# Performance work log

Hardware: AMD Instinct MI355X
Metric: run time of the kernel (lower is better)

The kernel has to match this reference:

```python
import jax, jax.numpy as jnp
import numpy as np
import math

B, C, T = 4, 512, 2048
H = 8            # num_heads
G = 32           # GroupNorm groups (GroupNorm32 in ADM-style code)
EPS = 1e-5


def setup_inputs() -> dict:
    key = jax.random.key(0)
    ks = jax.random.split(key, 7)
    x = jax.random.normal(ks[0], (B, C, T), jnp.float32)
    norm_scale = 1.0 + 0.02 * jax.random.normal(ks[1], (C,), jnp.float32)
    norm_bias = 0.02 * jax.random.normal(ks[2], (C,), jnp.float32)
    qkv_w = 0.02 * jax.random.normal(ks[3], (3 * C, C), jnp.float32)  # 1x1 conv == matmul
    qkv_b = 0.02 * jax.random.normal(ks[4], (3 * C,), jnp.float32)
    proj_w = 0.02 * jax.random.normal(ks[5], (C, C), jnp.float32)
    proj_b = 0.02 * jax.random.normal(ks[6], (C,), jnp.float32)
    return {"x": x, "norm_scale": norm_scale, "norm_bias": norm_bias,
            "qkv_w": qkv_w, "qkv_b": qkv_b, "proj_w": proj_w, "proj_b": proj_b}


def _group_norm(x, scale, bias):
    # x: [B, C, T]; 32-group norm over (C/G, T) per group
    b, c, t = x.shape
    xg = x.reshape(b, G, (c // G) * t)
    mean = jnp.mean(xg, axis=-1, keepdims=True)
    var = jnp.var(xg, axis=-1, keepdims=True)
    xg = (xg - mean) * jax.lax.rsqrt(var + EPS)
    return xg.reshape(b, c, t) * scale[None, :, None] + bias[None, :, None]


def reference(x, norm_scale, norm_bias, qkv_w, qkv_b, proj_w, proj_b):
    b, c, t = x.shape
    ch = c // H
    h = _group_norm(x, norm_scale, norm_bias)
    qkv = jnp.einsum('oc,bct->bot', qkv_w, h) + qkv_b[None, :, None]  # [B, 3C, T]
    q, k, v = jnp.split(qkv, 3, axis=1)
    q = q.reshape(b * H, ch, t)
    k = k.reshape(b * H, ch, t)
    v = v.reshape(b * H, ch, t)
    scale = 1.0 / math.sqrt(math.sqrt(ch))
    w = jnp.einsum('bct,bcs->bts', q * scale, k * scale)              # [B*H, T, T]
    w = jax.nn.softmax(w.astype(jnp.float32), axis=-1).astype(qkv.dtype)
    a = jnp.einsum('bts,bcs->bct', w, v).reshape(b, c, t)             # [B, C, T]
    out = jnp.einsum('oc,bct->bot', proj_w, a) + proj_b[None, :, None]
    return x + out
```

## Files before the change

### kernel.cpp

```cpp
#include <hip/hip_runtime.h>

typedef short bf16x8 __attribute__((ext_vector_type(8)));
typedef float f32x4 __attribute__((ext_vector_type(4)));
typedef float f32x16 __attribute__((ext_vector_type(16)));
typedef unsigned short u16;
typedef unsigned int u32;

constexpr int B = 4, C = 512, T = 2048, H = 8, G = 32;
constexpr int CH = C / H;
constexpr int CPG = C / G;
constexpr float EPS = 1e-5f;
constexpr float SCLQ = 0.18033688011112042f;

__device__ __forceinline__ u16 f2bf(float f) {
  union { float f; u32 u; } v; v.f = f;
  return (u16)((v.u + 0x7FFFu + ((v.u >> 16) & 1u)) >> 16);
}

__device__ __forceinline__ u32 cvtpk(float lo, float hi) {
  u32 r;
  asm("v_cvt_pk_bf16_f32 %0, %1, %2" : "=v"(r) : "v"(lo), "v"(hi));
  return r;
}

__device__ __forceinline__ void gload16(const void* g, void* lds) {
  __builtin_amdgcn_global_load_lds(
      (const __attribute__((address_space(1))) void*)g,
      (__attribute__((address_space(3))) void*)lds, 16, 0, 0);
}

__device__ __forceinline__ void pl32swap(u32& a, u32& b) {
  asm("v_permlane32_swap_b32 %0, %1" : "+v"(a), "+v"(b));
}

template <int ROWS>
__device__ __forceinline__ void stage_swz_8w(u16* lds, const u16* gsrc, int ldk) {
  const int tid = threadIdx.x;
  const int w = tid >> 6, lane = tid & 63;
#pragma unroll
  for (int i = 0; i < ROWS / 64; ++i) {
    const int chunk = i * 8 + w;
    const int row = chunk * 8 + (lane >> 3);
    const int col = ((lane & 7) * 8) ^ ((row & 7) << 3);
    gload16(gsrc + (size_t)row * ldk + col, (char*)lds + chunk * 1024);
  }
}

__global__ __launch_bounds__(256) void prep_k(const float* __restrict__ x,
                                              float* __restrict__ stats,
                                              const float* __restrict__ s1,
                                              u16* __restrict__ d1, int n1,
                                              const float* __restrict__ s2,
                                              u16* __restrict__ d2, int n2) {
  __shared__ float red[8];
  const int bid = blockIdx.x;
  if (bid >= 128) {
    int i = (bid - 128) * 256 + threadIdx.x;
    const float4* src = (const float4*)s1;
    uint2* dst = (uint2*)d1;
    float scl = (i < 65536) ? SCLQ : 1.0f;
    if (i >= n1) { i -= n1; scl = 1.0f; if (i >= n2) return; src = (const float4*)s2; dst = (uint2*)d2; }
    float4 v = src[i];
    uint2 pk;
    pk.x = cvtpk(v.x * scl, v.y * scl);
    pk.y = cvtpk(v.z * scl, v.w * scl);
    dst[i] = pk;
    return;
  }
  const int bg = bid;
  const float4* xp = (const float4*)(x + (size_t)bg * CPG * T);
  float s = 0.f, ss = 0.f;
  for (int i = threadIdx.x; i < CPG * T / 4; i += 256) {
    float4 v = xp[i];
    s += v.x + v.y + v.z + v.w;
    ss += v.x * v.x + v.y * v.y + v.z * v.z + v.w * v.w;
  }
  for (int off = 32; off; off >>= 1) {
    s += __shfl_down(s, off);
    ss += __shfl_down(ss, off);
  }
  const int w = threadIdx.x >> 6;
  if ((threadIdx.x & 63) == 0) { red[w] = s; red[4 + w] = ss; }
  __syncthreads();
  if (threadIdx.x == 0) {
    float S = red[0] + red[1] + red[2] + red[3];
    float SS = red[4] + red[5] + red[6] + red[7];
    const float inv = 1.f / (float)(CPG * T);
    float mean = S * inv;
    float var = SS * inv - mean * mean;
    stats[bg * 2] = mean;
    stats[bg * 2 + 1] = rsqrtf(var + EPS);
  }
}

__global__ __launch_bounds__(256) void gn_apply_k(const float* __restrict__ x,
                                                  const float* __restrict__ stats,
                                                  const float* __restrict__ gsc,
                                                  const float* __restrict__ gbi,
                                                  u16* __restrict__ ht) {
  const int b = blockIdx.y;
  const int t0 = blockIdx.x * 16;
#pragma unroll
  for (int p = 0; p < 2; ++p) {
    const int c = p * 256 + threadIdx.x;
    const int bg = b * G + (c >> 4);
    const float mean = stats[bg * 2], rstd = stats[bg * 2 + 1];
    const float sc = gsc[c] * rstd;
    const float bi = gbi[c] - mean * sc;
    const float4* xp = (const float4*)(x + ((size_t)b * C + c) * T + t0);
#pragma unroll
    for (int j = 0; j < 4; ++j) {
      float4 v = xp[j];
      const int t = t0 + j * 4;
      u16* hp = ht + ((size_t)b * T + t) * C + c;
      hp[0]     = f2bf(v.x * sc + bi);
      hp[C]     = f2bf(v.y * sc + bi);
      hp[2 * C] = f2bf(v.z * sc + bi);
      hp[3 * C] = f2bf(v.w * sc + bi);
    }
  }
}

__global__ __launch_bounds__(512, 2) void qkv_gemm_k(const u16* __restrict__ ht,
                                                     const u16* __restrict__ wq,
                                                     const float* __restrict__ qkvb,
                                                     u16* __restrict__ qo,
                                                     u16* __restrict__ kvo_k,
                                                     u16* __restrict__ kvo_v) {
  __shared__ u16 As[2][128 * 64];
  __shared__ u16 Bs[2][128 * 64];
  const int bid = blockIdx.x;
  const int wg = (bid & 7) * 96 + (bid >> 3);
  const int nt = wg % 12;
  const int mtb = wg / 12;
  const int mt = mtb & 15, b = mtb >> 4;
  const u16* Ab = ht + ((size_t)b * T + mt * 128) * C;
  const u16* Bb = wq + (size_t)nt * 128 * C;
  const int tid = threadIdx.x, lane = tid & 63, w = tid >> 6;
  const int wr = w >> 1, wc = w & 1, l15 = lane & 15, lhi = lane >> 4;
  const int swz = (l15 & 7) << 3;
  constexpr int NK = C / 64;

  const f32x4 vzero = {0.f, 0.f, 0.f, 0.f};
  f32x4 acc[2][4];
#pragma unroll
  for (int m = 0; m < 2; ++m)
#pragma unroll
    for (int n = 0; n < 4; ++n) acc[m][n] = vzero;

  stage_swz_8w<128>(As[0], Ab, C);
  stage_swz_8w<128>(Bs[0], Bb, C);
  asm volatile("s_waitcnt vmcnt(0)" ::: "memory");
  __builtin_amdgcn_s_barrier();
  asm volatile("" ::: "memory");

  int cur = 0;
  for (int kt = 0; kt < NK; ++kt) {
    if (kt + 1 < NK) {
      stage_swz_8w<128>(As[cur ^ 1], Ab + (kt + 1) * 64, C);
      stage_swz_8w<128>(Bs[cur ^ 1], Bb + (kt + 1) * 64, C);
    }
#pragma unroll
    for (int kk = 0; kk < 2; ++kk) {
      const int koff = (kk * 32 + lhi * 8) ^ swz;
      bf16x8 af[2], bfv[4];
#pragma unroll
      for (int m = 0; m < 2; ++m)
        af[m] = *(const bf16x8*)&As[cur][(wr * 32 + m * 16 + l15) * 64 + koff];
#pragma unroll
      for (int n = 0; n < 4; ++n)
        bfv[n] = *(const bf16x8*)&Bs[cur][(wc * 64 + n * 16 + l15) * 64 + koff];
#pragma unroll
      for (int m = 0; m < 2; ++m)
#pragma unroll
        for (int n = 0; n < 4; ++n)
          acc[m][n] = __builtin_amdgcn_mfma_f32_16x16x32_bf16(af[m], bfv[n], acc[m][n], 0, 0, 0);
    }
    if (kt + 1 < NK) {
      asm volatile("s_waitcnt vmcnt(0)" ::: "memory");
      __builtin_amdgcn_s_barrier();
      asm volatile("" ::: "memory");
    }
    cur ^= 1;
  }
#pragma unroll
  for (int n = 0; n < 4; ++n) {
    const int o = nt * 128 + wc * 64 + n * 16 + l15;
    const int which = o >> 9, rem = o & 511, hh = rem >> 6, d = rem & 63;
    const float bias = (which == 0) ? qkvb[o] * SCLQ : qkvb[o];
    const size_t bh = (size_t)b * H + hh;
#pragma unroll
    for (int m = 0; m < 2; ++m) {
      const int tbase = mt * 128 + wr * 32 + m * 16 + lhi * 4;
      const u32 w01 = cvtpk(acc[m][n][0] + bias, acc[m][n][1] + bias);
      const u32 w23 = cvtpk(acc[m][n][2] + bias, acc[m][n][3] + bias);
      if (which == 2) {
        uint2 pk; pk.x = w01; pk.y = w23;
        *(uint2*)&kvo_v[(bh * CH + d) * T + tbase] = pk;
      } else {
        u16* dst = (which == 0) ? qo : kvo_k;
        dst[(bh * T + tbase) * CH + d]     = (u16)(w01 & 0xffff);
        dst[(bh * T + tbase + 1) * CH + d] = (u16)(w01 >> 16);
        dst[(bh * T + tbase + 2) * CH + d] = (u16)(w23 & 0xffff);
        dst[(bh * T + tbase + 3) * CH + d] = (u16)(w23 >> 16);
      }
    }
  }
}

__global__ __launch_bounds__(512, 4) void attn_k(const u16* __restrict__ q,
                                                 const u16* __restrict__ k,
                                                 const u16* __restrict__ v,
                                                 u16* __restrict__ at) {
  __shared__ u16 Ks[2][128 * 64];
  __shared__ u16 Vs[2][2][64 * 64];
  const int lin = blockIdx.x + (blockIdx.y << 4);
  const int wg = (lin & 7) * 64 + (lin >> 3);
  const int qt = wg & 15, bh = wg >> 4;
  const int tid = threadIdx.x, lane = tid & 63, w = tid >> 6;
  const int qset = w & 3, grp = w >> 2;
  const int l31 = lane & 31, h = lane >> 5;
  const u16* qb = q + (size_t)bh * T * CH;
  const u16* kb = k + (size_t)bh * T * CH;
  const u16* vb = v + (size_t)bh * CH * T;
  constexpr int NP = T / 128;

  bf16x8 qf[4];
  {
    const u16* qp = qb + (size_t)(qt * 128 + qset * 32 + l31) * CH + h * 8;
#pragma unroll
    for (int ks = 0; ks < 4; ++ks) qf[ks] = *(const bf16x8*)(qp + ks * 16);
  }
  union { u32 u[4]; bf16x8 v8; } ones;
#pragma unroll
  for (int i = 0; i < 4; ++i) ones.u[i] = 0x3F803F80u;

  stage_swz_8w<128>(Ks[0], kb, CH);
  stage_swz_8w<64>(Vs[0][0], vb, T);
  stage_swz_8w<64>(Vs[0][1], vb + 64, T);
  asm volatile("s_waitcnt vmcnt(0)" ::: "memory");
  __builtin_amdgcn_s_barrier();
  asm volatile("" ::: "memory");

  f32x16 accO0 = {0.f,0.f,0.f,0.f,0.f,0.f,0.f,0.f,0.f,0.f,0.f,0.f,0.f,0.f,0.f,0.f};
  f32x16 accO1 = accO0;
  f32x16 accL = accO0;
  const int kswz = (l31 & 7) << 3;

  int cur = 0;
  for (int p = 0; p < NP; ++p) {
    if (p + 1 < NP) {
      stage_swz_8w<128>(Ks[cur ^ 1], kb + (size_t)(p + 1) * 128 * CH, CH);
      stage_swz_8w<64>(Vs[cur ^ 1][0], vb + (p + 1) * 128, T);
      stage_swz_8w<64>(Vs[cur ^ 1][1], vb + (p + 1) * 128 + 64, T);
    }
    const u16* Kc = &Ks[cur][grp * 64 * 64];
    const u16* Vc = Vs[cur][grp];

    f32x16 accS0 = {0.f,0.f,0.f,0.f,0.f,0.f,0.f,0.f,0.f,0.f,0.f,0.f,0.f,0.f,0.f,0.f};
    f32x16 accS1 = accS0;
    __builtin_amdgcn_s_setprio(1);
#pragma unroll
    for (int ks = 0; ks < 4; ++ks) {
      const int col = (ks * 16 + h * 8) ^ kswz;
      bf16x8 kf0 = *(const bf16x8*)&Kc[l31 * 64 + col];
      bf16x8 kf1 = *(const bf16x8*)&Kc[(32 + l31) * 64 + col];
      accS0 = __builtin_amdgcn_mfma_f32_32x32x16_bf16(kf0, qf[ks], accS0, 0, 0, 0);
      accS1 = __builtin_amdgcn_mfma_f32_32x32x16_bf16(kf1, qf[ks], accS1, 0, 0, 0);
    }
    __builtin_amdgcn_s_setprio(0);

    u32 wd0[8], wd1[8];
#pragma unroll
    for (int i = 0; i < 8; ++i) {
      float pa = __builtin_amdgcn_exp2f(accS0[2 * i]);
      float pb = __builtin_amdgcn_exp2f(accS0[2 * i + 1]);
      asm("v_cvt_pk_bf16_f32 %0, %1, %2" : "=v"(wd0[i]) : "v"(pa), "v"(pb));
    }
#pragma unroll
    for (int i = 0; i < 8; ++i) {
      float pa = __builtin_amdgcn_exp2f(accS1[2 * i]);
      float pb = __builtin_amdgcn_exp2f(accS1[2 * i + 1]);
      asm("v_cvt_pk_bf16_f32 %0, %1, %2" : "=v"(wd1[i]) : "v"(pa), "v"(pb));
    }
    pl32swap(wd0[0], wd0[2]); pl32swap(wd0[1], wd0[3]);
    pl32swap(wd0[4], wd0[6]); pl32swap(wd0[5], wd0[7]);
    pl32swap(wd1[0], wd1[2]); pl32swap(wd1[1], wd1[3]);
    pl32swap(wd1[4], wd1[6]); pl32swap(wd1[5], wd1[7]);

    __builtin_amdgcn_s_setprio(1);
#pragma unroll
    for (int kt = 0; kt < 2; ++kt) {
      const u32* wd = kt ? wd1 : wd0;
      union { u32 u[4]; bf16x8 v8; } fa, fb;
      fa.u[0] = wd[0]; fa.u[1] = wd[1]; fa.u[2] = wd[2]; fa.u[3] = wd[3];
      fb.u[0] = wd[4]; fb.u[1] = wd[5]; fb.u[2] = wd[6]; fb.u[3] = wd[7];
      const int sA = (kt * 32 + h * 8) ^ kswz;
      const int sB = (kt * 32 + 16 + h * 8) ^ kswz;
      {
        bf16x8 vf0 = *(const bf16x8*)&Vc[l31 * 64 + sA];
        bf16x8 vf1 = *(const bf16x8*)&Vc[l31 * 64 + sB];
        accO0 = __builtin_amdgcn_mfma_f32_32x32x16_bf16(fa.v8, vf0, accO0, 0, 0, 0);
        accO0 = __builtin_amdgcn_mfma_f32_32x32x16_bf16(fb.v8, vf1, accO0, 0, 0, 0);
      }
      {
        bf16x8 vf0 = *(const bf16x8*)&Vc[(32 + l31) * 64 + sA];
        bf16x8 vf1 = *(const bf16x8*)&Vc[(32 + l31) * 64 + sB];
        accO1 = __builtin_amdgcn_mfma_f32_32x32x16_bf16(fa.v8, vf0, accO1, 0, 0, 0);
        accO1 = __builtin_amdgcn_mfma_f32_32x32x16_bf16(fb.v8, vf1, accO1, 0, 0, 0);
      }
      accL = __builtin_amdgcn_mfma_f32_32x32x16_bf16(fa.v8, ones.v8, accL, 0, 0, 0);
      accL = __builtin_amdgcn_mfma_f32_32x32x16_bf16(fb.v8, ones.v8, accL, 0, 0, 0);
    }
    __builtin_amdgcn_s_setprio(0);

    asm volatile("s_waitcnt vmcnt(0)" ::: "memory");
    __builtin_amdgcn_s_barrier();
    asm volatile("" ::: "memory");
    cur ^= 1;
  }

  float* fO = (float*)&Ks[0][0];
  float* fL = (float*)&Vs[0][0][0];
  if (grp == 1) {
#pragma unroll
    for (int r = 0; r < 16; ++r) {
      const int qrow = (r & 3) + 8 * (r >> 2) + 4 * h;
      float* row = fO + (qset * 32 + qrow) * 64;
      row[l31] = accO0[r];
      row[32 + l31] = accO1[r];
      if (l31 == 0) fL[qset * 32 + qrow] = accL[r];
    }
  }
  __syncthreads();
  if (grp == 0) {
    const int bq = bh >> 3, hh = bh & 7;
#pragma unroll
    for (int r = 0; r < 16; ++r) {
      const int qrow = (r & 3) + 8 * (r >> 2) + 4 * h;
      const float denom = accL[r] + fL[qset * 32 + qrow];
      const float invr = __builtin_amdgcn_rcpf(denom);
      const float* row = fO + (qset * 32 + qrow) * 64;
      const float o0 = accO0[r] + row[l31];
      const float o1 = accO1[r] + row[32 + l31];
      const int t = qt * 128 + qset * 32 + qrow;
      u16* op = at + ((size_t)bq * T + t) * C + hh * 64 + l31;
      op[0]  = f2bf(o0 * invr);
      op[32] = f2bf(o1 * invr);
    }
  }
}

__global__ __launch_bounds__(512, 2) void proj_gemm_k(const u16* __restrict__ at,
                                                      const u16* __restrict__ wp,
                                                      const float* __restrict__ pb,
                                                      const float* __restrict__ x,
                                                      float* __restrict__ out) {
  __shared__ u16 As[2][128 * 64];
  __shared__ u16 Bs[2][64 * 64];
  const int bid = blockIdx.x;
  const int wg = (bid & 7) * 64 + (bid >> 3);
  const int nt = wg & 7;
  const int mtb = wg >> 3;
  const int mt = mtb & 15, b = mtb >> 4;
  const u16* Ab = at + ((size_t)b * T + mt * 128) * C;
  const u16* Bb = wp + (size_t)nt * 64 * C;
  const int tid = threadIdx.x, lane = tid & 63, w = tid >> 6;
  const int l15 = lane & 15, lhi = lane >> 4;
  const int swz = (l15 & 7) << 3;
  constexpr int NK = C / 64;

  const f32x4 vzero = {0.f, 0.f, 0.f, 0.f};
  f32x4 acc[4];
#pragma unroll
  for (int n = 0; n < 4; ++n) acc[n] = vzero;

  stage_swz_8w<128>(As[0], Ab, C);
  stage_swz_8w<64>(Bs[0], Bb, C);
  asm volatile("s_waitcnt vmcnt(0)" ::: "memory");
  __builtin_amdgcn_s_barrier();
  asm volatile("" ::: "memory");

  int cur = 0;
  for (int kt = 0; kt < NK; ++kt) {
    if (kt + 1 < NK) {
      stage_swz_8w<128>(As[cur ^ 1], Ab + (kt + 1) * 64, C);
      stage_swz_8w<64>(Bs[cur ^ 1], Bb + (kt + 1) * 64, C);
    }
#pragma unroll
    for (int kk = 0; kk < 2; ++kk) {
      const int koff = (kk * 32 + lhi * 8) ^ swz;
      bf16x8 af = *(const bf16x8*)&As[cur][(w * 16 + l15) * 64 + koff];
      bf16x8 bfv[4];
#pragma unroll
      for (int n = 0; n < 4; ++n)
        bfv[n] = *(const bf16x8*)&Bs[cur][(n * 16 + l15) * 64 + koff];
#pragma unroll
      for (int n = 0; n < 4; ++n)
        acc[n] = __builtin_amdgcn_mfma_f32_16x16x32_bf16(af, bfv[n], acc[n], 0, 0, 0);
    }
    if (kt + 1 < NK) {
      asm volatile("s_waitcnt vmcnt(0)" ::: "memory");
      __builtin_amdgcn_s_barrier();
      asm volatile("" ::: "memory");
    }
    cur ^= 1;
  }
#pragma unroll
  for (int n = 0; n < 4; ++n) {
    const int o = nt * 64 + n * 16 + l15;
    const float bias = pb[o];
    const int tbase = mt * 128 + w * 16 + lhi * 4;
    const size_t idx = ((size_t)b * C + o) * T + tbase;
    const float4 xv = *(const float4*)&x[idx];
    float4 ov;
    ov.x = xv.x + acc[n][0] + bias;
    ov.y = xv.y + acc[n][1] + bias;
    ov.z = xv.z + acc[n][2] + bias;
    ov.w = xv.w + acc[n][3] + bias;
    *(float4*)&out[idx] = ov;
  }
}

extern "C" void kernel_launch(void* const* d_in, const int* in_sizes, int n_in,
                              void* d_out, int out_size, void* d_ws, size_t ws_size,
                              hipStream_t stream) {
  const float* x     = (const float*)d_in[0];
  const float* gsc   = (const float*)d_in[1];
  const float* gbi   = (const float*)d_in[2];
  const float* qkvw  = (const float*)d_in[3];
  const float* qkvb  = (const float*)d_in[4];
  const float* projw = (const float*)d_in[5];
  const float* projb = (const float*)d_in[6];
  float* out = (float*)d_out;

  char* ws = (char*)d_ws;
  float* stats = (float*)ws;
  u16* wq = (u16*)(ws + 1024);
  u16* wp = (u16*)(ws + 1024 + 1572864);
  u16* ht = (u16*)(ws + 2098176);
  u16* qo = (u16*)(ws + 10486784);
  u16* ko = (u16*)(ws + 18875392);
  u16* vo = (u16*)(ws + 27264000);
  u16* at = ht;

  prep_k<<<1152, 256, 0, stream>>>(x, stats, qkvw, wq, 196608, projw, wp, 65536);
  gn_apply_k<<<dim3(T / 16, B), 256, 0, stream>>>(x, stats, gsc, gbi, ht);
  qkv_gemm_k<<<768, 512, 0, stream>>>(ht, wq, qkvb, qo, ko, vo);
  attn_k<<<dim3(T / 128, B * H), 512, 0, stream>>>(qo, ko, vo, at);
  proj_gemm_k<<<512, 512, 0, stream>>>(at, wp, projb, x, out);
}
```

Measured before the change: 104.7 us.

## Software-pipeline QK^T one tile ahead of softmax and PV in attention loop

Restructures the attention main loop so the S=K·Q MFMAs for tile p+1 are issued after the exp/convert of tile p and before the PV MFMAs. K is now prefetched two tiles ahead and V one tile ahead, with a prologue that computes the first S tile. The aim is to overlap the transcendental/VALU softmax work with matrix-core work and keep the MFMA pipe busy. In exchange the S accumulators stay live across iterations, which raises register pressure, and the extra prologue barrier adds a little synchronization.

```diff
diff --git a/kernel.cpp b/kernel.cpp
--- a/kernel.cpp
+++ b/kernel.cpp
@@ -238,37 +238,39 @@
   stage_swz_8w<128>(Ks[0], kb, CH);
   stage_swz_8w<64>(Vs[0][0], vb, T);
   stage_swz_8w<64>(Vs[0][1], vb + 64, T);
+  stage_swz_8w<128>(Ks[1], kb + (size_t)128 * CH, CH);
   asm volatile("s_waitcnt vmcnt(0)" ::: "memory");
   __builtin_amdgcn_s_barrier();
   asm volatile("" ::: "memory");
 
-  f32x16 accO0 = {0.f,0.f,0.f,0.f,0.f,0.f,0.f,0.f,0.f,0.f,0.f,0.f,0.f,0.f,0.f,0.f};
-  f32x16 accO1 = accO0;
-  f32x16 accL = accO0;
+  const f32x16 fz = {0.f,0.f,0.f,0.f,0.f,0.f,0.f,0.f,0.f,0.f,0.f,0.f,0.f,0.f,0.f,0.f};
+  f32x16 accO0 = fz, accO1 = fz, accL = fz;
+  f32x16 accS0, accS1;
   const int kswz = (l31 & 7) << 3;
 
-  int cur = 0;
-  for (int p = 0; p < NP; ++p) {
-    if (p + 1 < NP) {
-      stage_swz_8w<128>(Ks[cur ^ 1], kb + (size_t)(p + 1) * 128 * CH, CH);
-      stage_swz_8w<64>(Vs[cur ^ 1][0], vb + (p + 1) * 128, T);
-      stage_swz_8w<64>(Vs[cur ^ 1][1], vb + (p + 1) * 128 + 64, T);
-    }
-    const u16* Kc = &Ks[cur][grp * 64 * 64];
-    const u16* Vc = Vs[cur][grp];
-
-    f32x16 accS0 = {0.f,0.f,0.f,0.f,0.f,0.f,0.f,0.f,0.f,0.f,0.f,0.f,0.f,0.f,0.f,0.f};
-    f32x16 accS1 = accS0;
+  {
+    const u16* Kc = &Ks[0][grp * 64 * 64];
     __builtin_amdgcn_s_setprio(1);
 #pragma unroll
     for (int ks = 0; ks < 4; ++ks) {
       const int col = (ks * 16 + h * 8) ^ kswz;
       bf16x8 kf0 = *(const bf16x8*)&Kc[l31 * 64 + col];
       bf16x8 kf1 = *(const bf16x8*)&Kc[(32 + l31) * 64 + col];
-      accS0 = __builtin_amdgcn_mfma_f32_32x32x16_bf16(kf0, qf[ks], accS0, 0, 0, 0);
-      accS1 = __builtin_amdgcn_mfma_f32_32x32x16_bf16(kf1, qf[ks], accS1, 0, 0, 0);
+      accS0 = __builtin_amdgcn_mfma_f32_32x32x16_bf16(kf0, qf[ks], ks == 0 ? fz : accS0, 0, 0, 0);
+      accS1 = __builtin_amdgcn_mfma_f32_32x32x16_bf16(kf1, qf[ks], ks == 0 ? fz : accS1, 0, 0, 0);
     }
     __builtin_amdgcn_s_setprio(0);
+  }
+  __builtin_amdgcn_s_barrier();
+  asm volatile("" ::: "memory");
+
+  for (int p = 0; p < NP; ++p) {
+    if (p + 2 < NP)
+      stage_swz_8w<128>(Ks[p & 1], kb + (size_t)(p + 2) * 128 * CH, CH);
+    if (p + 1 < NP) {
+      stage_swz_8w<64>(Vs[(p + 1) & 1][0], vb + (p + 1) * 128, T);
+      stage_swz_8w<64>(Vs[(p + 1) & 1][1], vb + (p + 1) * 128 + 64, T);
+    }
 
     u32 wd0[8], wd1[8];
 #pragma unroll
@@ -288,6 +290,21 @@
     pl32swap(wd1[0], wd1[2]); pl32swap(wd1[1], wd1[3]);
     pl32swap(wd1[4], wd1[6]); pl32swap(wd1[5], wd1[7]);
 
+    if (p + 1 < NP) {
+      const u16* Kc = &Ks[(p + 1) & 1][grp * 64 * 64];
+      __builtin_amdgcn_s_setprio(1);
+#pragma unroll
+      for (int ks = 0; ks < 4; ++ks) {
+        const int col = (ks * 16 + h * 8) ^ kswz;
+        bf16x8 kf0 = *(const bf16x8*)&Kc[l31 * 64 + col];
+        bf16x8 kf1 = *(const bf16x8*)&Kc[(32 + l31) * 64 + col];
+        accS0 = __builtin_amdgcn_mfma_f32_32x32x16_bf16(kf0, qf[ks], ks == 0 ? fz : accS0, 0, 0, 0);
+        accS1 = __builtin_amdgcn_mfma_f32_32x32x16_bf16(kf1, qf[ks], ks == 0 ? fz : accS1, 0, 0, 0);
+      }
+      __builtin_amdgcn_s_setprio(0);
+    }
+
+    const u16* Vc = Vs[p & 1][grp];
     __builtin_amdgcn_s_setprio(1);
 #pragma unroll
     for (int kt = 0; kt < 2; ++kt) {
@@ -317,7 +334,6 @@
     asm volatile("s_waitcnt vmcnt(0)" ::: "memory");
     __builtin_amdgcn_s_barrier();
     asm volatile("" ::: "memory");
-    cur ^= 1;
   }
 
   float* fO = (float*)&Ks[0][0];
```

New measurement: 119.3 us. 14.0% more time.
